# Optimization experiments

Measured on AMD Instinct MI355X. Metric: run time of the kernel, lower is better.

## Reference

```python
import jax, jax.numpy as jnp
import numpy as np

EPS = 1e-5
K = 20
LRELU = 0.2


def _bn(x, g, b, ch_axis):
    # inference BatchNorm with running_mean=0, running_var=1
    shape = [1] * x.ndim
    shape[ch_axis] = -1
    scale = (g / jnp.sqrt(1.0 + EPS)).reshape(shape)
    bias = b.reshape(shape)
    return x * scale + bias


def _lrelu(x):
    return jnp.where(x > 0, x, LRELU * x)


def _edge_conv(x, W, g, b):
    # x: (B, C, N) -> (B, C_out, N)
    B, C, N = x.shape
    xt = jnp.swapaxes(x, 1, 2)                      # (B, N, C)
    inner = -2.0 * jnp.einsum('bnc,bmc->bnm', xt, xt)
    xx = jnp.sum(xt * xt, axis=2)                   # (B, N)
    pdist = -xx[:, :, None] - inner - xx[:, None, :]  # negative sq dist (B,N,N)
    idx = jax.lax.top_k(pdist, K)[1]                # (B, N, K) nearest (incl. self)
    # gather neighbor features per batch: (C, N) indexed by (N, K) -> (C, N, K)
    neighbors = jax.vmap(lambda xf, id_: xf[:, id_])(x, idx)  # (B, C, N, K)
    center = jnp.broadcast_to(x[..., None], (B, C, N, K))
    edge = jnp.concatenate([center, neighbors - center], axis=1)  # (B, 2C, N, K)
    h = jnp.einsum('oc,bcnk->bonk', W, edge)        # 1x1 conv, no bias
    h = _lrelu(_bn(h, g, b, 1))
    return jnp.max(h, axis=-1)                      # (B, C_out, N)


def setup_inputs() -> dict:
    key = jax.random.key(0)
    ks = jax.random.split(key, 24)
    B, N = 4, 2048
    d = {}
    d['points'] = jax.random.normal(ks[0], (B, N, 3), dtype=jnp.float32)

    def w(k_, shape):
        return 0.1 * jax.random.normal(k_, shape, dtype=jnp.float32)

    def gam(k_, c):
        return 1.0 + 0.1 * jax.random.normal(k_, (c,), dtype=jnp.float32)

    def bet(k_, c):
        return 0.05 * jax.random.normal(k_, (c,), dtype=jnp.float32)

    # EdgeConv blocks: (out, 2*in)
    d['w1'], d['g1'], d['b1'] = w(ks[1], (64, 6)), gam(ks[2], 64), bet(ks[3], 64)
    d['w2'], d['g2'], d['b2'] = w(ks[4], (64, 128)), gam(ks[5], 64), bet(ks[6], 64)
    d['w3'], d['g3'], d['b3'] = w(ks[7], (128, 128)), gam(ks[8], 128), bet(ks[9], 128)
    d['w4'], d['g4'], d['b4'] = w(ks[10], (256, 256)), gam(ks[11], 256), bet(ks[12], 256)
    # conv5 1x1: 512 -> 1024
    d['w5'], d['g5'], d['b5'] = w(ks[13], (1024, 512)), gam(ks[14], 1024), bet(ks[15], 1024)
    # fc: 2048 -> 512 -> 256
    d['fw1'], d['fb1'] = w(ks[16], (512, 2048)), 0.05 * jax.random.normal(ks[17], (512,), dtype=jnp.float32)
    d['g6'], d['b6'] = gam(ks[18], 512), bet(ks[19], 512)
    d['fw2'], d['fb2'] = w(ks[20], (256, 512)), 0.05 * jax.random.normal(ks[21], (256,), dtype=jnp.float32)
    d['g7'], d['b7'] = gam(ks[22], 256), bet(ks[23], 256)
    return d


def reference(points, w1, g1, b1, w2, g2, b2, w3, g3, b3, w4, g4, b4,
              w5, g5, b5, fw1, fb1, g6, b6, fw2, fb2, g7, b7):
    x = jnp.swapaxes(points[:, :, :3], 1, 2)        # (B, 3, N)
    x1 = _edge_conv(x, w1, g1, b1)                  # (B, 64, N)
    x2 = _edge_conv(x1, w2, g2, b2)                 # (B, 64, N)
    x3 = _edge_conv(x2, w3, g3, b3)                 # (B, 128, N)
    x4 = _edge_conv(x3, w4, g4, b4)                 # (B, 256, N)
    h = jnp.concatenate([x1, x2, x3, x4], axis=1)   # (B, 512, N)
    h = _lrelu(_bn(jnp.einsum('oc,bcn->bon', w5, h), g5, b5, 1))  # (B, 1024, N)
    h_max = jnp.max(h, axis=-1)
    h_avg = jnp.mean(h, axis=-1)
    f = jnp.concatenate([h_max, h_avg], axis=1)     # (B, 2048)
    f = _lrelu(_bn(f @ fw1.T + fb1, g6, b6, 1))     # dropout = identity (eval)
    f = _bn(f @ fw2.T + fb2, g7, b7, 1)
    return f                                        # (B, 256)
```

## Files before the change

### kernel.cpp

```cpp
#include <hip/hip_runtime.h>
#include <hip/hip_bf16.h>
#include <float.h>

#define N_PTS 2048
#define B_SZ  4
#define KNN   20
#define LRELU_S 0.2f
#define FT    512
#define NPOOL 8

typedef __hip_bfloat16 bf16;
typedef __attribute__((ext_vector_type(8))) short short8v;
typedef __attribute__((ext_vector_type(4))) float floatx4;

__device__ __forceinline__ float b2f(const bf16 v) { return __bfloat162float(v); }
__device__ __forceinline__ float ldf(const float* p) { return *p; }
__device__ __forceinline__ float ldf(const bf16* p)  { return __bfloat162float(*p); }
__device__ __forceinline__ short8v ld8(const bf16* p) { return *(const short8v*)p; }
__device__ __forceinline__ unsigned umin(unsigned a, unsigned b) { return a < b ? a : b; }

__device__ __forceinline__ void gload16(const void* g, void* l) {
    __builtin_amdgcn_global_load_lds(
        (const __attribute__((address_space(1))) void*)g,
        (__attribute__((address_space(3))) void*)l, 16, 0, 0);
}

__global__ void k_sniff(const unsigned short* __restrict__ pts_hw, int* __restrict__ flag) {
    if (threadIdx.x != 0 || blockIdx.x != 0) return;
    int sane = 0;
    for (int j = 0; j < 64; ++j) {
        unsigned short v = pts_hw[2 * j];
        int e = (v >> 7) & 0xFF;
        if (e >= 100 && e <= 140) ++sane;
    }
    *flag = (sane >= 32) ? 1 : 0;
}

struct WPack {
    const void* src[23];
    int off[24];
    int rows[23];
    int cols[23];
};

__global__ void k_repack(WPack wp, const int* __restrict__ flag, float* __restrict__ dst, int limit) {
    const int isb = *flag;
    int i = blockIdx.x * blockDim.x + threadIdx.x;
    if (i >= limit) return;
    int lo = 0, hi = 23;
    while (lo + 1 < hi) { int mid = (lo + hi) >> 1; if (i >= wp.off[mid]) lo = mid; else hi = mid; }
    int j = i - wp.off[lo];
    float v = isb ? b2f(((const bf16*)wp.src[lo])[j]) : ((const float*)wp.src[lo])[j];
    int dj = j;
    int cols = wp.cols[lo];
    if (cols) dj = (j % cols) * wp.rows[lo] + (j / cols);
    dst[wp.off[lo] + dj] = v;
}

template<int C, int COUT>
__global__ void k_wsplit(const void* __restrict__ W, const int* __restrict__ flag,
                         bf16* __restrict__ dst) {
    int i = blockIdx.x * blockDim.x + threadIdx.x;
    if (i >= COUT * C) return;
    int o = i / C, c = i % C;
    const int isb = *flag;
    float w1 = isb ? b2f(((const bf16*)W)[(size_t)o * 2 * C + c])
                   : ((const float*)W)[(size_t)o * 2 * C + c];
    float w2 = isb ? b2f(((const bf16*)W)[(size_t)o * 2 * C + C + c])
                   : ((const float*)W)[(size_t)o * 2 * C + C + c];
    float wd = w1 - w2;
    bf16 h2 = __float2bfloat16(w2);
    bf16 hd = __float2bfloat16(wd);
    dst[i]                = h2;
    dst[COUT * C + i]     = __float2bfloat16(w2 - b2f(h2));
    dst[2 * COUT * C + i] = hd;
    dst[3 * COUT * C + i] = __float2bfloat16(wd - b2f(hd));
}

__global__ void k_w5split(const void* __restrict__ W, const int* __restrict__ flag,
                          bf16* __restrict__ dst) {
    int i = blockIdx.x * blockDim.x + threadIdx.x;
    if (i >= 1024 * 512) return;
    const int isb = *flag;
    float w = isb ? b2f(((const bf16*)W)[i]) : ((const float*)W)[i];
    bf16 h = __float2bfloat16(w);
    dst[i] = h;
    dst[1024 * 512 + i] = __float2bfloat16(w - b2f(h));
}

__global__ void k_transpose(const void* __restrict__ pts, const int* __restrict__ flag,
                            float* __restrict__ x0) {
    const int isb = *flag;
    int i = blockIdx.x * blockDim.x + threadIdx.x;
    if (i >= B_SZ * N_PTS) return;
    int b = i / N_PTS, n = i % N_PTS;
    for (int c = 0; c < 3; ++c) {
        size_t s = ((size_t)b * N_PTS + n) * 3 + c;
        float v = isb ? b2f(((const bf16*)pts)[s]) : ((const float*)pts)[s];
        x0[((size_t)b * 3 + c) * N_PTS + n] = v;
    }
}

__device__ __forceinline__ void load32(const float* row, int mbase, float* r) {
    const float4* p = (const float4*)(row + mbase);
#pragma unroll
    for (int i = 0; i < 8; ++i) {
        float4 f = p[i];
        r[4 * i + 0] = f.x; r[4 * i + 1] = f.y; r[4 * i + 2] = f.z; r[4 * i + 3] = f.w;
    }
}
__device__ __forceinline__ void load32(const bf16* row, int mbase, float* r) {
    const uint4* p = (const uint4*)(row + mbase);
#pragma unroll
    for (int i = 0; i < 4; ++i) {
        uint4 u = p[i];
        r[8 * i + 0] = __uint_as_float(u.x << 16);
        r[8 * i + 1] = __uint_as_float(u.x & 0xFFFF0000u);
        r[8 * i + 2] = __uint_as_float(u.y << 16);
        r[8 * i + 3] = __uint_as_float(u.y & 0xFFFF0000u);
        r[8 * i + 4] = __uint_as_float(u.z << 16);
        r[8 * i + 5] = __uint_as_float(u.z & 0xFFFF0000u);
        r[8 * i + 6] = __uint_as_float(u.w << 16);
        r[8 * i + 7] = __uint_as_float(u.w & 0xFFFF0000u);
    }
}

__device__ __forceinline__ void s2ins(unsigned k, unsigned& m1, unsigned& m2) {
    unsigned lo = umin(m1, k);
    unsigned hi = (m1 < k) ? k : m1;
    m1 = lo;
    m2 = umin(m2, hi);
}

__device__ __forceinline__ void select20x2(const unsigned* ka, const unsigned* kb,
                                           int* outA, int* outB, int lane) {
    const unsigned SENT = 0xFFFFFFFFu;
    unsigned a1 = SENT, a2 = SENT, b1 = SENT, b2 = SENT;
#pragma unroll
    for (int j = 0; j < 32; ++j) {
        s2ins(ka[j], a1, a2);
        s2ins(kb[j], b1, b2);
    }
#pragma unroll 1
    for (int k = 0; k < KNN; ++k) {
        unsigned va = a1, vb = b1;
#pragma unroll
        for (int off = 32; off >= 1; off >>= 1) {
            va = umin(va, (unsigned)__shfl_xor((int)va, off));
            vb = umin(vb, (unsigned)__shfl_xor((int)vb, off));
        }
        if (lane == 0) { outA[k] = (int)(va & 2047u); outB[k] = (int)(vb & 2047u); }
        if (a1 == va) { a1 = a2; a2 = SENT; }
        if (b1 == vb) { b1 = b2; b2 = SENT; }
        if (a1 == SENT) {
#pragma unroll
            for (int j = 0; j < 32; ++j) {
                unsigned t = (ka[j] > va) ? ka[j] : SENT;
                s2ins(t, a1, a2);
            }
        }
        if (b1 == SENT) {
#pragma unroll
            for (int j = 0; j < 32; ++j) {
                unsigned t = (kb[j] > vb) ? kb[j] : SENT;
                s2ins(t, b1, b2);
            }
        }
    }
}

__global__ __launch_bounds__(256) void k_knn3(const float* __restrict__ x0,
                                              int* __restrict__ idx) {
    __shared__ float qf[8][3];
    int ib = blockIdx.x;
    int b  = ib / (N_PTS / 8);
    int q0 = (ib % (N_PTS / 8)) * 8;
    const float* xb = x0 + (size_t)b * 3 * N_PTS;

    if (threadIdx.x < 24) {
        int q = threadIdx.x / 3, c = threadIdx.x % 3;
        qf[q][c] = xb[(size_t)c * N_PTS + q0 + q];
    }
    __syncthreads();
// ... 40 lines not shown
    float xqa = xr[qa], xqb = xr[qa + 1];

    unsigned ka[32], kb[32];
#pragma unroll
    for (int r = 0; r < 8; ++r) {
        int m0 = r * 256 + (lane << 2);
        float4 x4 = *(const float4*)(xr + m0);
        float4 a4 = *(const float4*)(gA + m0);
        float4 b4 = *(const float4*)(gB + m0);
        float s;
        s = fmaf(-2.f, a4.x, x4.x) + xqa; s = fmaxf(s, 0.f);
        ka[4 * r + 0] = (__float_as_uint(s) & 0xFFFFF800u) | (unsigned)(m0 + 0);
        s = fmaf(-2.f, a4.y, x4.y) + xqa; s = fmaxf(s, 0.f);
        ka[4 * r + 1] = (__float_as_uint(s) & 0xFFFFF800u) | (unsigned)(m0 + 1);
        s = fmaf(-2.f, a4.z, x4.z) + xqa; s = fmaxf(s, 0.f);
        ka[4 * r + 2] = (__float_as_uint(s) & 0xFFFFF800u) | (unsigned)(m0 + 2);
        s = fmaf(-2.f, a4.w, x4.w) + xqa; s = fmaxf(s, 0.f);
        ka[4 * r + 3] = (__float_as_uint(s) & 0xFFFFF800u) | (unsigned)(m0 + 3);
        s = fmaf(-2.f, b4.x, x4.x) + xqb; s = fmaxf(s, 0.f);
        kb[4 * r + 0] = (__float_as_uint(s) & 0xFFFFF800u) | (unsigned)(m0 + 0);
        s = fmaf(-2.f, b4.y, x4.y) + xqb; s = fmaxf(s, 0.f);
        kb[4 * r + 1] = (__float_as_uint(s) & 0xFFFFF800u) | (unsigned)(m0 + 1);
        s = fmaf(-2.f, b4.z, x4.z) + xqb; s = fmaxf(s, 0.f);
        kb[4 * r + 2] = (__float_as_uint(s) & 0xFFFFF800u) | (unsigned)(m0 + 2);
        s = fmaf(-2.f, b4.w, x4.w) + xqb; s = fmaxf(s, 0.f);
        kb[4 * r + 3] = (__float_as_uint(s) & 0xFFFFF800u) | (unsigned)(m0 + 3);
    }
    select20x2(ka, kb, idx + ((size_t)b * N_PTS + qa) * KNN,
               idx + ((size_t)b * N_PTS + qa + 1) * KNN, lane);
}

template<typename T, int C>
__global__ __launch_bounds__(256) void k_knn(const T* __restrict__ x, int bstride,
                                             int* __restrict__ idx) {
    __shared__ float qf[4][C];
    int ib = blockIdx.x;
    int b  = ib / (N_PTS / 4);
    int q0 = (ib % (N_PTS / 4)) * 4;
    const T* xb = x + (size_t)b * bstride;

    for (int t = threadIdx.x; t < 4 * C; t += 256) {
        int pt = t / C, c = t % C;
        qf[pt][c] = ldf(&xb[(size_t)c * N_PTS + (q0 + pt)]);
    }
    __syncthreads();

    int w = threadIdx.x >> 6, lane = threadIdx.x & 63;
    int q = q0 + w;
    int mbase = lane * 32;

    float v[32];
#pragma unroll
    for (int j = 0; j < 32; ++j) v[j] = 0.f;

    for (int c = 0; c < C; ++c) {
        float qc = qf[w][c];
        float r[32];
        load32(xb + (size_t)c * N_PTS, mbase, r);
#pragma unroll
        for (int j = 0; j < 32; ++j) { float t = r[j] - qc; v[j] = fmaf(t, t, v[j]); }
    }

    for (int k = 0; k < KNN; ++k) {
        float bv = FLT_MAX; int bi = 0x7FFFFFFF;
#pragma unroll
        for (int j = 0; j < 32; ++j)
            if (v[j] < bv) { bv = v[j]; bi = mbase + j; }
#pragma unroll
        for (int off = 32; off >= 1; off >>= 1) {
            float ov = __shfl_xor(bv, off);
            int   oi = __shfl_xor(bi, off);
            if (ov < bv || (ov == bv && oi < bi)) { bv = ov; bi = oi; }
        }
        if (lane == 0) idx[((size_t)b * N_PTS + q) * KNN + k] = bi;
        int wl = bi >> 5, wj = bi & 31;
        if (lane == wl) {
#pragma unroll
            for (int j = 0; j < 32; ++j) if (j == wj) v[j] = FLT_MAX;
        }
    }
}

template<int C>
__global__ void k_xx(const bf16* __restrict__ featT, int c0, float* __restrict__ xx) {
    int i = blockIdx.x * blockDim.x + threadIdx.x;
    if (i >= B_SZ * N_PTS) return;
    const bf16* row = featT + (size_t)i * FT + c0;
    float s = 0.f;
    for (int c = 0; c < C; c += 8) {
        uint4 u = *(const uint4*)(row + c);
        float v0 = __uint_as_float(u.x << 16), v1 = __uint_as_float(u.x & 0xFFFF0000u);
        float v2 = __uint_as_float(u.y << 16), v3 = __uint_as_float(u.y & 0xFFFF0000u);
        float v4 = __uint_as_float(u.z << 16), v5 = __uint_as_float(u.z & 0xFFFF0000u);
        float v6 = __uint_as_float(u.w << 16), v7 = __uint_as_float(u.w & 0xFFFF0000u);
        s = fmaf(v0, v0, s); s = fmaf(v1, v1, s); s = fmaf(v2, v2, s); s = fmaf(v3, v3, s);
        s = fmaf(v4, v4, s); s = fmaf(v5, v5, s); s = fmaf(v6, v6, s); s = fmaf(v7, v7, s);
    }
    xx[i] = s;
}

template<int C>
__global__ __launch_bounds__(256) void k_gram(const bf16* __restrict__ featT, int c0,
                                              float* __restrict__ G) {
    const int KC = 64;
    __shared__ __align__(16) short At[128 * 64];
    __shared__ __align__(16) short Bt[128 * 64];

    int ib = blockIdx.x;
    int b  = ib >> 8;
    int t  = ib & 255;
    int n0 = (t >> 4) << 7;
    int m0 = (t & 15) << 7;

    int tid = threadIdx.x;
    int w = tid >> 6, lane = tid & 63;
    int rw = (w & 1) * 64, cw = (w >> 1) * 64;
    int lrow = lane & 15, quad = lane >> 4;

    floatx4 acc[4][4];
#pragma unroll
    for (int ri = 0; ri < 4; ++ri)
#pragma unroll
        for (int ci = 0; ci < 4; ++ci) acc[ri][ci] = (floatx4){0.f, 0.f, 0.f, 0.f};

    for (int ck = 0; ck < C; ck += KC) {
        __syncthreads();
#pragma unroll
        for (int it = 0; it < 4; ++it) {
            int s = tid + it * 256;
            int row = s >> 3, seg = s & 7;
            int gseg = seg ^ (row & 7);
            gload16(featT + ((size_t)(b * N_PTS + n0 + row) * FT) + c0 + ck + gseg * 8,
                    &At[(s & ~63) * 8]);
            gload16(featT + ((size_t)(b * N_PTS + m0 + row) * FT) + c0 + ck + gseg * 8,
                    &Bt[(s & ~63) * 8]);
        }
        __syncthreads();
#pragma unroll
        for (int kk = 0; kk < KC; kk += 32) {
            int ks = kk >> 3;
            short8v a[4], bb[4];
#pragma unroll
            for (int ri = 0; ri < 4; ++ri) {
                int row = rw + ri * 16 + lrow;
                int seg = (ks + quad) ^ (row & 7);
                a[ri] = *(const short8v*)&At[row * 64 + seg * 8];
            }
#pragma unroll
            for (int ci = 0; ci < 4; ++ci) {
                int row = cw + ci * 16 + lrow;
                int seg = (ks + quad) ^ (row & 7);
                bb[ci] = *(const short8v*)&Bt[row * 64 + seg * 8];
            }
#pragma unroll
            for (int ri = 0; ri < 4; ++ri)
#pragma unroll
                for (int ci = 0; ci < 4; ++ci)
                    acc[ri][ci] = __builtin_amdgcn_mfma_f32_16x16x32_bf16(a[ri], bb[ci], acc[ri][ci], 0, 0, 0);
        }
    }

#pragma unroll
    for (int ri = 0; ri < 4; ++ri)
#pragma unroll
        for (int ci = 0; ci < 4; ++ci) {
            int n = n0 + rw + ri * 16 + quad * 4;
            int m = m0 + cw + ci * 16 + lrow;
            float* gp = G + ((size_t)b * N_PTS + n) * N_PTS + m;
#pragma unroll
            for (int reg = 0; reg < 4; ++reg)
                gp[(size_t)reg * N_PTS] = acc[ri][ci][reg];
        }
}

template<int COUT, int C>
__global__ __launch_bounds__(256) void k_xform(const bf16* __restrict__ featT, int c0,
                                               const bf16* __restrict__ Wsp,
                                               float* __restrict__ Y) {
    const int M2 = 2 * COUT;
    const int KC = 64;
    __shared__ __align__(16) short Bt[128 * 64];

    int ib = blockIdx.x;
    int nt = ib & 63;
    int mt = ib >> 6;
    int tid = threadIdx.x;
    int w = tid >> 6, lane = tid & 63;
    int rw = (w & 1) * 64, cw = (w >> 1) * 64;
    int l15 = lane & 15, quad = lane >> 4;

    floatx4 acc[4][4];
#pragma unroll
    for (int ri = 0; ri < 4; ++ri)
#pragma unroll
        for (int ci = 0; ci < 4; ++ci) acc[ri][ci] = (floatx4){0.f, 0.f, 0.f, 0.f};

    for (int ck = 0; ck < C; ck += KC) {
        __syncthreads();
#pragma unroll
        for (int it = 0; it < 4; ++it) {
            int s = tid + it * 256;
            int row = s >> 3, seg = s & 7;
            int gseg = seg ^ (row & 7);
            gload16(featT + (size_t)(nt * 128 + row) * FT + c0 + ck + gseg * 8,
                    &Bt[(s & ~63) * 8]);
        }
        __syncthreads();
#pragma unroll
        for (int kk = 0; kk < KC; kk += 32) {
            int ks = kk >> 3;
            short8v bfr[4];
#pragma unroll
            for (int ci = 0; ci < 4; ++ci) {
                int row = cw + ci * 16 + l15;
                int seg = (ks + quad) ^ (row & 7);
                bfr[ci] = *(const short8v*)&Bt[row * 64 + seg * 8];
            }
#pragma unroll
            for (int ri = 0; ri < 4; ++ri) {
                int mrow = mt * 128 + rw + ri * 16 + l15;
                int base = (mrow < COUT) ? mrow : (mrow + COUT);
                const bf16* hi = Wsp + (size_t)base * C + ck + kk + quad * 8;
                short8v ah = ld8(hi);
                short8v al = ld8(hi + (size_t)COUT * C);
#pragma unroll
                for (int ci = 0; ci < 4; ++ci) {
                    acc[ri][ci] = __builtin_amdgcn_mfma_f32_16x16x32_bf16(ah, bfr[ci], acc[ri][ci], 0, 0, 0);
                    acc[ri][ci] = __builtin_amdgcn_mfma_f32_16x16x32_bf16(al, bfr[ci], acc[ri][ci], 0, 0, 0);
                }
            }
        }
    }

#pragma unroll
    for (int ri = 0; ri < 4; ++ri)
#pragma unroll
        for (int ci = 0; ci < 4; ++ci) {
            int n = nt * 128 + cw + ci * 16 + l15;
            int m = mt * 128 + rw + ri * 16 + quad * 4;
            *(floatx4*)(Y + (size_t)n * M2 + m) = acc[ri][ci];
        }
}

template<int COUT>
__global__ __launch_bounds__(256) void k_gmax(const float* __restrict__ Y,
        const int* __restrict__ idx,
        const float* __restrict__ gam, const float* __restrict__ bet,
        bf16* __restrict__ featT, int c0f) {
    const int M2 = 2 * COUT;
    const int OT = COUT / 64;
    int i = blockIdx.x * 4 + (threadIdx.x >> 6);
    int lane = threadIdx.x & 63;
    int b = i >> 11;

    const float inv = rsqrtf(1.0f + 1e-5f);
    float yd[OT], scale[OT], bias[OT], mx[OT];
#pragma unroll
    for (int j = 0; j < OT; ++j) {
        int o = lane + 64 * j;
        yd[j]    = Y[(size_t)i * M2 + COUT + o];
        scale[j] = gam[o] * inv;
        bias[j]  = bet[o];
        mx[j]    = -FLT_MAX;
    }

    const int* ip = idx + (size_t)i * KNN;
    const float* Yb = Y + ((size_t)b * N_PTS) * M2;
#pragma unroll 4
    for (int k = 0; k < KNN; ++k) {
        int m = ip[k] & (N_PTS - 1);
        const float* yr = Yb + (size_t)m * M2;
#pragma unroll
        for (int j = 0; j < OT; ++j) {
            float h = (yd[j] + yr[lane + 64 * j]) * scale[j] + bias[j];
            h = h > 0.f ? h : LRELU_S * h;
            mx[j] = fmaxf(mx[j], h);
        }
    }
#pragma unroll
    for (int j = 0; j < OT; ++j)
        featT[(size_t)i * FT + c0f + lane + 64 * j] = __float2bfloat16(mx[j]);
}

template<typename T, int C, int COUT, bool WF>
__global__ __launch_bounds__(256) void k_edgeconv(const T* __restrict__ x, int bstride,
                           const int* __restrict__ idx,
                           const float* __restrict__ Wt,
                           const float* __restrict__ gam,
                           const float* __restrict__ bet,
                           bf16* __restrict__ out, int ostride,
                           bf16* __restrict__ featT, int c0f) {
    const int PT = 4;
    const int OT = COUT / 64;
    const int CP = (C + 3) & ~3;
    __shared__ float sh[PT][KNN + 1][CP];

    int ib = blockIdx.x;
    int b  = ib / (N_PTS / PT);
    int n0 = (ib % (N_PTS / PT)) * PT;
    const T* xb = x + (size_t)b * bstride;

    const int TOT = PT * (KNN + 1) * C;
    for (int t = threadIdx.x; t < TOT; t += 256) {
        int pt = t / ((KNN + 1) * C);
        int r  = t % ((KNN + 1) * C);
        int row = r / C, c = r % C;
        int n = n0 + pt;
        int m = (row == 0) ? n
                           : (idx[((size_t)b * N_PTS + n) * KNN + (row - 1)] & (N_PTS - 1));
        sh[pt][row][c] = ldf(&xb[(size_t)c * N_PTS + m]);
    }
    __syncthreads();

    int w = threadIdx.x >> 6, lane = threadIdx.x & 63;
    int n = n0 + w;

    constexpr int KT = (OT >= 4) ? 10 : 20;
    constexpr int NPASS = KNN / KT;

    float base[OT];
    float mx[OT];
#pragma unroll
    for (int j = 0; j < OT; ++j) { base[j] = 0.f; mx[j] = -FLT_MAX; }

    const float inv = rsqrtf(1.0f + 1e-5f);

#pragma unroll
    for (int pass = 0; pass < NPASS; ++pass) {
        float acc[OT][KT];
#pragma unroll
        for (int j = 0; j < OT; ++j)
#pragma unroll
            for (int k = 0; k < KT; ++k) acc[j][k] = 0.f;

        for (int c = 0; c < C; ++c) {
            float xq = sh[w][0][c];
            float w2v[OT];
#pragma unroll
            for (int j = 0; j < OT; ++j)
                w2v[j] = Wt[(size_t)(C + c) * COUT + lane + 64 * j];
            if (pass == 0) {
#pragma unroll
                for (int j = 0; j < OT; ++j) {
                    float w1v = Wt[(size_t)c * COUT + lane + 64 * j];
                    base[j] = fmaf(w1v - w2v[j], xq, base[j]);
                }
            }
#pragma unroll
            for (int k = 0; k < KT; ++k) {
                float nv = sh[w][1 + pass * KT + k][c];
#pragma unroll
                for (int j = 0; j < OT; ++j) acc[j][k] = fmaf(w2v[j], nv, acc[j][k]);
            }
        }

#pragma unroll
        for (int j = 0; j < OT; ++j) {
            int o = lane + 64 * j;
            float scale = gam[o] * inv, bias = bet[o];
#pragma unroll
            for (int k = 0; k < KT; ++k) {
                float h = (base[j] + acc[j][k]) * scale + bias;
                h = h > 0.f ? h : LRELU_S * h;
                mx[j] = fmaxf(mx[j], h);
            }
        }
    }

#pragma unroll
    for (int j = 0; j < OT; ++j) {
        int o = lane + 64 * j;
        bf16 bv = __float2bfloat16(mx[j]);
        out[(size_t)b * ostride + (size_t)o * N_PTS + n] = bv;
        if (WF) featT[((size_t)b * N_PTS + n) * FT + c0f + o] = bv;
    }
}

__global__ __launch_bounds__(256) void k_conv5mfma(
        const bf16* __restrict__ featT, const bf16* __restrict__ w5sp,
        const float* __restrict__ g5, const float* __restrict__ b5,
        float* __restrict__ fmxp, float* __restrict__ fsmp) {
    __shared__ __align__(16) short Bt[256 * 64];
    __shared__ __align__(16) short Ah[64 * 64];
    __shared__ __align__(16) short Al[64 * 64];
    __shared__ float rmx[4][64];
    __shared__ float rsm[4][64];

    int ib = blockIdx.x;
    int b  = ib / 128;
    int rem = ib % 128;
    int o0 = (rem >> 3) * 64;
    int nt = rem & 7;
    int tid = threadIdx.x;
    int w = tid >> 6, lane = tid & 63;
    int l15 = lane & 15, quad = lane >> 4;

    const bf16* Whi = w5sp;
    const bf16* Wlo = w5sp + 1024 * 512;
    const bf16* fb  = featT + (size_t)b * N_PTS * FT;
    const int nbase0 = nt * 256;

    floatx4 acc[4][4];
#pragma unroll
    for (int mi = 0; mi < 4; ++mi)
#pragma unroll
        for (int ni = 0; ni < 4; ++ni) acc[mi][ni] = (floatx4){0.f, 0.f, 0.f, 0.f};

    for (int ck = 0; ck < 512; ck += 64) {
        __syncthreads();
#pragma unroll
        for (int it = 0; it < 8; ++it) {
            int s = tid + it * 256;
            int row = s >> 3, seg = s & 7;
            int gseg = seg ^ (row & 7);
            gload16(fb + (size_t)(nbase0 + row) * FT + ck + gseg * 8,
                    &Bt[(s & ~63) * 8]);
        }
#pragma unroll
        for (int it = 0; it < 2; ++it) {
            int s = tid + it * 256;
            int row = s >> 3, seg = s & 7;
            int gseg = seg ^ (row & 7);
            gload16(Whi + (size_t)(o0 + row) * 512 + ck + gseg * 8, &Ah[(s & ~63) * 8]);
            gload16(Wlo + (size_t)(o0 + row) * 512 + ck + gseg * 8, &Al[(s & ~63) * 8]);
        }
        __syncthreads();
#pragma unroll
        for (int kk = 0; kk < 64; kk += 32) {
            int ks = kk >> 3;
            short8v bfr[4], ah[4], al[4];
#pragma unroll
            for (int ni = 0; ni < 4; ++ni) {
                int row = w * 64 + ni * 16 + l15;
                int seg = (ks + quad) ^ (row & 7);
                bfr[ni] = *(const short8v*)&Bt[row * 64 + seg * 8];
            }
#pragma unroll
            for (int mi = 0; mi < 4; ++mi) {
                int row = mi * 16 + l15;
                int seg = (ks + quad) ^ (row & 7);
                ah[mi] = *(const short8v*)&Ah[row * 64 + seg * 8];
                al[mi] = *(const short8v*)&Al[row * 64 + seg * 8];
            }
#pragma unroll
            for (int mi = 0; mi < 4; ++mi)
#pragma unroll
                for (int ni = 0; ni < 4; ++ni) {
                    acc[mi][ni] = __builtin_amdgcn_mfma_f32_16x16x32_bf16(ah[mi], bfr[ni], acc[mi][ni], 0, 0, 0);
                    acc[mi][ni] = __builtin_amdgcn_mfma_f32_16x16x32_bf16(al[mi], bfr[ni], acc[mi][ni], 0, 0, 0);
                }
        }
    }

    const float inv = rsqrtf(1.0f + 1e-5f);
#pragma unroll
    for (int mi = 0; mi < 4; ++mi) {
#pragma unroll
        for (int r = 0; r < 4; ++r) {
            int o = o0 + mi * 16 + quad * 4 + r;
            float scale = g5[o] * inv, bias = b5[o];
            float mx = -FLT_MAX, sm = 0.f;
#pragma unroll
            for (int ni = 0; ni < 4; ++ni) {
                float h = acc[mi][ni][r] * scale + bias;
                h = h > 0.f ? h : LRELU_S * h;
                mx = fmaxf(mx, h);
                sm += h;
            }
#pragma unroll
            for (int off = 1; off <= 8; off <<= 1) {
                mx = fmaxf(mx, __shfl_xor(mx, off));
                sm += __shfl_xor(sm, off);
            }
            if (l15 == 0) {
                rmx[w][mi * 16 + quad * 4 + r] = mx;
                rsm[w][mi * 16 + quad * 4 + r] = sm;
            }
        }
    }
    __syncthreads();
    if (tid < 64) {
        float mx = -FLT_MAX, sm = 0.f;
#pragma unroll
        for (int ww = 0; ww < 4; ++ww) { mx = fmaxf(mx, rmx[ww][tid]); sm += rsm[ww][tid]; }
        fmxp[((size_t)b * 1024 + o0 + tid) * NPOOL + nt] = mx;
        fsmp[((size_t)b * 1024 + o0 + tid) * NPOOL + nt] = sm;
    }
}

__global__ void k_pool(const float* __restrict__ fmxp, const float* __restrict__ fsmp,
                       float* __restrict__ fvec) {
    int i = blockIdx.x * blockDim.x + threadIdx.x;
    if (i >= B_SZ * 1024) return;
    int b = i >> 10, o = i & 1023;
    float mx = -FLT_MAX, sm = 0.f;
    for (int ch = 0; ch < NPOOL; ++ch) {
        mx = fmaxf(mx, fmxp[(size_t)i * NPOOL + ch]);
        sm += fsmp[(size_t)i * NPOOL + ch];
    }
    fvec[(size_t)b * 2048 + o] = mx;
    fvec[(size_t)b * 2048 + 1024 + o] = sm * (1.0f / N_PTS);
}

__global__ __launch_bounds__(256) void k_fc1(const float* __restrict__ fvec,
        const void* __restrict__ fw1, const void* __restrict__ fb1,
        const void* __restrict__ g6,  const void* __restrict__ b6,
        const int* __restrict__ flag, float* __restrict__ tbuf) {
    __shared__ float red[4];
    int ib = blockIdx.x;
    int b = ib >> 9, o = ib & 511;
    const float* fv = fvec + (size_t)b * 2048;
    int tid = threadIdx.x;
    const int isb = *flag;
    float s = 0.f;
    if (isb) {
        const bf16* wr = (const bf16*)fw1 + (size_t)o * 2048;
        for (int j = tid; j < 2048; j += 256) s = fmaf(b2f(wr[j]), fv[j], s);
    } else {
        const float* wr = (const float*)fw1 + (size_t)o * 2048;
        for (int j = tid; j < 2048; j += 256) s = fmaf(wr[j], fv[j], s);
    }
#pragma unroll
    for (int off = 32; off >= 1; off >>= 1) s += __shfl_xor(s, off);
    if ((tid & 63) == 0) red[tid >> 6] = s;
    __syncthreads();
    if (tid == 0) {
        float fb = isb ? b2f(((const bf16*)fb1)[o]) : ((const float*)fb1)[o];
        float gg = isb ? b2f(((const bf16*)g6)[o])  : ((const float*)g6)[o];
        float bb = isb ? b2f(((const bf16*)b6)[o])  : ((const float*)b6)[o];
        float acc = fb + red[0] + red[1] + red[2] + red[3];
        float h = acc * gg * rsqrtf(1.0f + 1e-5f) + bb;
        tbuf[(size_t)b * 512 + o] = h > 0.f ? h : LRELU_S * h;
// ... 142 lines not shown
    __syncthreads();
    const float inv = rsqrtf(1.0f + 1e-5f);
    for (int o = threadIdx.x; o < 512; o += 256) {
        const float* wr = fw1 + (size_t)o * 2048;
        float acc = fb1[o];
        for (int j = 0; j < 2048; ++j) acc += wr[j] * f[j];
        float h = acc * g6[o] * inv + b6[o];
        t[o] = h > 0.f ? h : LRELU_S * h;
    }
    __syncthreads();
    {
        int o = threadIdx.x;
        const float* wr = fw2 + (size_t)o * 512;
        float acc = fb2[o];
        for (int j = 0; j < 512; ++j) acc += wr[j] * t[j];
        float h = acc * g7[o] * inv + b7[o];
        if (*flag) ((bf16*)out)[(size_t)b * 256 + o] = __float2bfloat16(h);
        else       ((float*)out)[(size_t)b * 256 + o] = h;
    }
}

extern "C" void kernel_launch(void* const* d_in, const int* in_sizes, int n_in,
                              void* d_out, int out_size, void* d_ws, size_t ws_size,
                              hipStream_t stream) {
    static const int wsz[23] = {
        384, 64, 64,   8192, 64, 64,   16384, 128, 128,   65536, 256, 256,
        524288, 1024, 1024,   1048576, 512,   512, 512,   131072, 256,   256, 256
    };
    static const int trows[23] = {64,0,0, 64,0,0, 128,0,0, 256,0,0, 0,0,0, 0,0, 0,0, 0,0, 0,0};
    static const int tcols[23] = { 6,0,0,128,0,0, 128,0,0, 256,0,0, 0,0,0, 0,0, 0,0, 0,0, 0,0};

    WPack wp;
    int total = 0;
    for (int i = 0; i < 23; ++i) {
        wp.src[i] = d_in[i + 1]; wp.off[i] = total; total += wsz[i];
        wp.rows[i] = trows[i]; wp.cols[i] = tcols[i];
    }
    wp.off[23] = total;

    const size_t flag_bytes = 16;
    const size_t x0_bytes   = (size_t)B_SZ * 3 * N_PTS * 4;
    const size_t feat_bytes = (size_t)B_SZ * 512 * N_PTS * 2;
    const size_t idx_bytes  = (size_t)B_SZ * N_PTS * KNN * 4;
    const size_t pool_bytes = (size_t)B_SZ * 1024 * 4 * 2;
    const size_t wf_bytes   = (size_t)total * 4;
    const size_t base_need  = flag_bytes + x0_bytes + feat_bytes + idx_bytes + pool_bytes + wf_bytes;

    const size_t featT_bytes = (size_t)B_SZ * N_PTS * FT * 2;
    const size_t xx_bytes    = (size_t)B_SZ * N_PTS * 4;
    const size_t wsp2_elems  = 4 * 64 * 64;
    const size_t wsp3_elems  = 4 * 128 * 64;
    const size_t wsp4_elems  = 4 * 256 * 128;
    const size_t w5sp_elems  = 2 * 1024 * 512;
    const size_t wsp_bytes   = (wsp2_elems + wsp3_elems + wsp4_elems + w5sp_elems) * 2;
    const size_t S_bytes     = (size_t)B_SZ * N_PTS * N_PTS * 4;
    const size_t full_need   = base_need + featT_bytes + xx_bytes + wsp_bytes + S_bytes;

    if (ws_size < base_need) return;
    const bool use_gram = (ws_size >= full_need);

    char* w = (char*)d_ws;
    int*   flag = (int*)w;              w += flag_bytes;
    float* x0   = (float*)w;            w += x0_bytes;
    bf16*  feat = (bf16*)w;             w += feat_bytes;
    int*   idx  = (int*)w;              w += idx_bytes;
    w += pool_bytes;
    float* wf   = (float*)w;            w += wf_bytes;
    bf16*  featT = (bf16*)w;            w += featT_bytes;
    float* xx    = (float*)w;           w += xx_bytes;
    bf16*  wsp2  = (bf16*)w;            w += wsp2_elems * 2;
    bf16*  wsp3  = (bf16*)w;            w += wsp3_elems * 2;
    bf16*  wsp4  = (bf16*)w;            w += wsp4_elems * 2;
    bf16*  w5sp  = (bf16*)w;            w += w5sp_elems * 2;
    float* S     = (float*)w;

    float* fmxp = (float*)idx;
    float* fsmp = fmxp + (size_t)B_SZ * 1024 * NPOOL;
    float* fvec = fsmp + (size_t)B_SZ * 1024 * NPOOL;
    float* tbuf = fvec + (size_t)B_SZ * 2048;

    const int FBS = 512 * N_PTS;

    k_sniff<<<1, 64, 0, stream>>>((const unsigned short*)d_in[0], flag);
    const int rlimit = use_gram ? wp.off[15] : total;
    k_repack<<<(rlimit + 255) / 256, 256, 0, stream>>>(wp, flag, wf, rlimit);
    k_transpose<<<(B_SZ * N_PTS + 255) / 256, 256, 0, stream>>>(d_in[0], flag, x0);

    const float* w1t = wf + wp.off[0],  *g1 = wf + wp.off[1],  *b1 = wf + wp.off[2];
    const float* w2t = wf + wp.off[3],  *g2 = wf + wp.off[4],  *b2 = wf + wp.off[5];
    const float* w3t = wf + wp.off[6],  *g3 = wf + wp.off[7],  *b3 = wf + wp.off[8];
    const float* w4t = wf + wp.off[9],  *g4 = wf + wp.off[10], *b4 = wf + wp.off[11];
    const float* w5  = wf + wp.off[12], *g5 = wf + wp.off[13], *b5 = wf + wp.off[14];
    const float* fw1 = wf + wp.off[15], *fb1 = wf + wp.off[16];
    const float* g6  = wf + wp.off[17], *b6 = wf + wp.off[18];
    const float* fw2 = wf + wp.off[19], *fb2 = wf + wp.off[20];
    const float* g7  = wf + wp.off[21], *b7 = wf + wp.off[22];

    const int GK = B_SZ * N_PTS / 4;
    const int G8 = B_SZ * N_PTS / 8;
    const int NXX = (B_SZ * N_PTS + 255) / 256;

    if (use_gram) {
        k_wsplit<64, 64><<<(64 * 64 + 255) / 256, 256, 0, stream>>>(d_in[4], flag, wsp2);
        k_wsplit<64, 128><<<(128 * 64 + 255) / 256, 256, 0, stream>>>(d_in[7], flag, wsp3);
        k_wsplit<128, 256><<<(256 * 128 + 255) / 256, 256, 0, stream>>>(d_in[10], flag, wsp4);
        k_w5split<<<(1024 * 512 + 255) / 256, 256, 0, stream>>>(d_in[13], flag, w5sp);

        k_knn3<<<G8, 256, 0, stream>>>(x0, idx);
        k_edgeconv<float, 3, 64, true><<<GK, 256, 0, stream>>>(
            x0, 3 * N_PTS, idx, w1t, g1, b1, feat + 0 * N_PTS, FBS, featT, 0);
        k_xx<64><<<NXX, 256, 0, stream>>>(featT, 0, xx);
        k_gram<64><<<B_SZ * 256, 256, 0, stream>>>(featT, 0, S);
        k_select2<<<G8, 256, 0, stream>>>(S, xx, idx);
        k_xform<64, 64><<<64, 256, 0, stream>>>(featT, 0, wsp2, S);
        k_gmax<64><<<GK, 256, 0, stream>>>(S, idx, g2, b2, featT, 64);
        k_xx<64><<<NXX, 256, 0, stream>>>(featT, 64, xx);
        k_gram<64><<<B_SZ * 256, 256, 0, stream>>>(featT, 64, S);
        k_select2<<<G8, 256, 0, stream>>>(S, xx, idx);
        k_xform<128, 64><<<128, 256, 0, stream>>>(featT, 64, wsp3, S);
        k_gmax<128><<<GK, 256, 0, stream>>>(S, idx, g3, b3, featT, 128);
        k_xx<128><<<NXX, 256, 0, stream>>>(featT, 128, xx);
        k_gram<128><<<B_SZ * 256, 256, 0, stream>>>(featT, 128, S);
        k_select2<<<G8, 256, 0, stream>>>(S, xx, idx);
        k_xform<256, 128><<<256, 256, 0, stream>>>(featT, 128, wsp4, S);
        k_gmax<256><<<GK, 256, 0, stream>>>(S, idx, g4, b4, featT, 256);

        k_conv5mfma<<<B_SZ * 128, 256, 0, stream>>>(featT, w5sp, g5, b5, fmxp, fsmp);
        k_pool<<<(B_SZ * 1024 + 255) / 256, 256, 0, stream>>>(fmxp, fsmp, fvec);
        k_fc1<<<B_SZ * 512, 256, 0, stream>>>(fvec, d_in[16], d_in[17], d_in[18], d_in[19],
                                              flag, tbuf);
        k_fc2<<<B_SZ * 256, 256, 0, stream>>>(tbuf, d_in[20], d_in[21], d_in[22], d_in[23],
                                              flag, d_out);
    } else {
        k_knn<float, 3><<<GK, 256, 0, stream>>>(x0, 3 * N_PTS, idx);
        k_edgeconv<float, 3, 64, false><<<GK, 256, 0, stream>>>(
            x0, 3 * N_PTS, idx, w1t, g1, b1, feat + 0 * N_PTS, FBS, nullptr, 0);
        k_knn<bf16, 64><<<GK, 256, 0, stream>>>(feat + 0 * N_PTS, FBS, idx);
        k_edgeconv<bf16, 64, 64, false><<<GK, 256, 0, stream>>>(
            feat + 0 * N_PTS, FBS, idx, w2t, g2, b2, feat + 64 * N_PTS, FBS, nullptr, 0);
        k_knn<bf16, 64><<<GK, 256, 0, stream>>>(feat + 64 * N_PTS, FBS, idx);
        k_edgeconv<bf16, 64, 128, false><<<GK, 256, 0, stream>>>(
            feat + 64 * N_PTS, FBS, idx, w3t, g3, b3, feat + 128 * N_PTS, FBS, nullptr, 0);
        k_knn<bf16, 128><<<GK, 256, 0, stream>>>(feat + 128 * N_PTS, FBS, idx);
        k_edgeconv<bf16, 128, 256, false><<<GK, 256, 0, stream>>>(
            feat + 128 * N_PTS, FBS, idx, w4t, g4, b4, feat + 256 * N_PTS, FBS, nullptr, 0);

        k_conv5pool<<<B_SZ * (1024 / 8) * NCH, 256, 0, stream>>>(feat, w5, g5, b5, fmxp, fsmp);
        k_head<<<B_SZ, 256, 0, stream>>>(fmxp, fsmp, fw1, fb1, g6, b6, fw2, fb2, g7, b7,
                                         flag, d_out);
    }
}
```

Before: 401.8 us.

## Merge prep kernels, fold squared-norm into producers, skip lo-weight MFMAs for bf16 input

Six weight-repack, split and transpose launches become one multi-role prep kernel. The separate k_xx squared-norm kernels are removed; the norms are now computed from the rounded bf16 outputs inside edgeconv and gmax via a wave reduction. When the input is detected as bf16, the low-order weight half is exactly zero, so xform and conv5 skip those loads and extra MFMAs. This cuts launch count, one pass over featT per layer, and about half the matrix work on the bf16 path, at the cost of a runtime branch on the flag.

```diff
diff --git a/kernel.cpp b/kernel.cpp
--- a/kernel.cpp
+++ b/kernel.cpp
@@ -43,9 +43,8 @@
     int cols[23];
 };
 
-__global__ void k_repack(WPack wp, const int* __restrict__ flag, float* __restrict__ dst, int limit) {
-    const int isb = *flag;
-    int i = blockIdx.x * blockDim.x + threadIdx.x;
+__device__ __forceinline__ void repack_body(const WPack& wp, int isb,
+                                            float* __restrict__ dst, int i, int limit) {
     if (i >= limit) return;
     int lo = 0, hi = 23;
     while (lo + 1 < hi) { int mid = (lo + hi) >> 1; if (i >= wp.off[mid]) lo = mid; else hi = mid; }
@@ -58,12 +57,10 @@
 }
 
 template<int C, int COUT>
-__global__ void k_wsplit(const void* __restrict__ W, const int* __restrict__ flag,
-                         bf16* __restrict__ dst) {
-    int i = blockIdx.x * blockDim.x + threadIdx.x;
+__device__ __forceinline__ void wsplit_body(const void* __restrict__ W, int isb,
+                                            bf16* __restrict__ dst, int i) {
     if (i >= COUT * C) return;
     int o = i / C, c = i % C;
-    const int isb = *flag;
     float w1 = isb ? b2f(((const bf16*)W)[(size_t)o * 2 * C + c])
                    : ((const float*)W)[(size_t)o * 2 * C + c];
     float w2 = isb ? b2f(((const bf16*)W)[(size_t)o * 2 * C + C + c])
@@ -77,21 +74,17 @@
     dst[3 * COUT * C + i] = __float2bfloat16(wd - b2f(hd));
 }
 
-__global__ void k_w5split(const void* __restrict__ W, const int* __restrict__ flag,
-                          bf16* __restrict__ dst) {
-    int i = blockIdx.x * blockDim.x + threadIdx.x;
+__device__ __forceinline__ void w5split_body(const void* __restrict__ W, int isb,
+                                             bf16* __restrict__ dst, int i) {
     if (i >= 1024 * 512) return;
-    const int isb = *flag;
     float w = isb ? b2f(((const bf16*)W)[i]) : ((const float*)W)[i];
     bf16 h = __float2bfloat16(w);
     dst[i] = h;
     dst[1024 * 512 + i] = __float2bfloat16(w - b2f(h));
 }
 
-__global__ void k_transpose(const void* __restrict__ pts, const int* __restrict__ flag,
-                            float* __restrict__ x0) {
-    const int isb = *flag;
-    int i = blockIdx.x * blockDim.x + threadIdx.x;
+__device__ __forceinline__ void transpose_body(const void* __restrict__ pts, int isb,
+                                               float* __restrict__ x0, int i) {
     if (i >= B_SZ * N_PTS) return;
     int b = i / N_PTS, n = i % N_PTS;
     for (int c = 0; c < 3; ++c) {
@@ -99,6 +92,37 @@
         float v = isb ? b2f(((const bf16*)pts)[s]) : ((const float*)pts)[s];
         x0[((size_t)b * 3 + c) * N_PTS + n] = v;
     }
+}
+
+__global__ void k_prep(WPack wp, const int* __restrict__ flag, float* __restrict__ wf,
+                       int rlimit,
+                       const void* __restrict__ w2s, bf16* __restrict__ wsp2,
+                       const void* __restrict__ w3s, bf16* __restrict__ wsp3,
+                       const void* __restrict__ w4s, bf16* __restrict__ wsp4,
+                       const void* __restrict__ w5s, bf16* __restrict__ w5sp,
+                       const void* __restrict__ pts, float* __restrict__ x0) {
+    const int isb = *flag;
+    const int nbrep = (rlimit + 255) >> 8;
+    int ib = blockIdx.x, t = threadIdx.x;
+    if (ib < nbrep) { repack_body(wp, isb, wf, ib * 256 + t, rlimit); return; }
+    ib -= nbrep;
+    if (ib < 16)   { wsplit_body<64, 64>(w2s, isb, wsp2, ib * 256 + t); return; }
+    ib -= 16;
+    if (ib < 32)   { wsplit_body<64, 128>(w3s, isb, wsp3, ib * 256 + t); return; }
+    ib -= 32;
+    if (ib < 128)  { wsplit_body<128, 256>(w4s, isb, wsp4, ib * 256 + t); return; }
+    ib -= 128;
+    if (ib < 2048) { w5split_body(w5s, isb, w5sp, ib * 256 + t); return; }
+    ib -= 2048;
+    transpose_body(pts, isb, x0, ib * 256 + t);
+}
+
+__global__ void k_repack(WPack wp, const int* __restrict__ flag, float* __restrict__ dst, int limit) {
+    repack_body(wp, *flag, dst, blockIdx.x * blockDim.x + threadIdx.x, limit);
+}
+__global__ void k_transpose(const void* __restrict__ pts, const int* __restrict__ flag,
+                            float* __restrict__ x0) {
+    transpose_body(pts, *flag, x0, blockIdx.x * blockDim.x + threadIdx.x);
 }
 
 __device__ __forceinline__ void load32(const float* row, int mbase, float* r) {
@@ -305,24 +329,6 @@
 }
 
 template<int C>
-__global__ void k_xx(const bf16* __restrict__ featT, int c0, float* __restrict__ xx) {
-    int i = blockIdx.x * blockDim.x + threadIdx.x;
-    if (i >= B_SZ * N_PTS) return;
-    const bf16* row = featT + (size_t)i * FT + c0;
-    float s = 0.f;
-    for (int c = 0; c < C; c += 8) {
-        uint4 u = *(const uint4*)(row + c);
-        float v0 = __uint_as_float(u.x << 16), v1 = __uint_as_float(u.x & 0xFFFF0000u);
-        float v2 = __uint_as_float(u.y << 16), v3 = __uint_as_float(u.y & 0xFFFF0000u);
-        float v4 = __uint_as_float(u.z << 16), v5 = __uint_as_float(u.z & 0xFFFF0000u);
-        float v6 = __uint_as_float(u.w << 16), v7 = __uint_as_float(u.w & 0xFFFF0000u);
-        s = fmaf(v0, v0, s); s = fmaf(v1, v1, s); s = fmaf(v2, v2, s); s = fmaf(v3, v3, s);
-        s = fmaf(v4, v4, s); s = fmaf(v5, v5, s); s = fmaf(v6, v6, s); s = fmaf(v7, v7, s);
-    }
-    xx[i] = s;
-}
-
-template<int C>
 __global__ __launch_bounds__(256) void k_gram(const bf16* __restrict__ featT, int c0,
                                               float* __restrict__ G) {
     const int KC = 64;
@@ -399,11 +405,13 @@
 template<int COUT, int C>
 __global__ __launch_bounds__(256) void k_xform(const bf16* __restrict__ featT, int c0,
                                                const bf16* __restrict__ Wsp,
-                                               float* __restrict__ Y) {
+                                               float* __restrict__ Y,
+                                               const int* __restrict__ flag) {
     const int M2 = 2 * COUT;
     const int KC = 64;
     __shared__ __align__(16) short Bt[128 * 64];
 
+    const int isb = *flag;
     int ib = blockIdx.x;
     int nt = ib & 63;
     int mt = ib >> 6;
@@ -441,15 +449,19 @@
             }
 #pragma unroll
             for (int ri = 0; ri < 4; ++ri) {
-                int mrow = mt * 128 + rw + ri * 16 + l15;
+                int rbase = mt * 128 + rw + ri * 16;
+                bool uselo = (!isb) || (rbase >= COUT);
+                int mrow = rbase + l15;
                 int base = (mrow < COUT) ? mrow : (mrow + COUT);
                 const bf16* hi = Wsp + (size_t)base * C + ck + kk + quad * 8;
                 short8v ah = ld8(hi);
-                short8v al = ld8(hi + (size_t)COUT * C);
+                short8v al;
+                if (uselo) al = ld8(hi + (size_t)COUT * C);
 #pragma unroll
                 for (int ci = 0; ci < 4; ++ci) {
                     acc[ri][ci] = __builtin_amdgcn_mfma_f32_16x16x32_bf16(ah, bfr[ci], acc[ri][ci], 0, 0, 0);
-                    acc[ri][ci] = __builtin_amdgcn_mfma_f32_16x16x32_bf16(al, bfr[ci], acc[ri][ci], 0, 0, 0);
+                    if (uselo)
+                        acc[ri][ci] = __builtin_amdgcn_mfma_f32_16x16x32_bf16(al, bfr[ci], acc[ri][ci], 0, 0, 0);
                 }
             }
         }
@@ -469,7 +481,7 @@
 __global__ __launch_bounds__(256) void k_gmax(const float* __restrict__ Y,
         const int* __restrict__ idx,
         const float* __restrict__ gam, const float* __restrict__ bet,
-        bf16* __restrict__ featT, int c0f) {
+        bf16* __restrict__ featT, int c0f, float* __restrict__ xxout) {
     const int M2 = 2 * COUT;
     const int OT = COUT / 64;
     int i = blockIdx.x * 4 + (threadIdx.x >> 6);
@@ -500,9 +512,18 @@
             mx[j] = fmaxf(mx[j], h);
         }
     }
-#pragma unroll
-    for (int j = 0; j < OT; ++j)
-        featT[(size_t)i * FT + c0f + lane + 64 * j] = __float2bfloat16(mx[j]);
+    float s = 0.f;
+#pragma unroll
+    for (int j = 0; j < OT; ++j) {
+        bf16 bv = __float2bfloat16(mx[j]);
+        featT[(size_t)i * FT + c0f + lane + 64 * j] = bv;
+        if (xxout) { float q = b2f(bv); s = fmaf(q, q, s); }
+    }
+    if (xxout) {
+#pragma unroll
+        for (int off = 32; off >= 1; off >>= 1) s += __shfl_xor(s, off);
+        if (lane == 0) xxout[i] = s;
+    }
 }
 
 template<typename T, int C, int COUT, bool WF>
@@ -512,7 +533,8 @@
                            const float* __restrict__ gam,
                            const float* __restrict__ bet,
                            bf16* __restrict__ out, int ostride,
-                           bf16* __restrict__ featT, int c0f) {
+                           bf16* __restrict__ featT, int c0f,
+                           float* __restrict__ xxout) {
     const int PT = 4;
     const int OT = COUT / 64;
     const int CP = (C + 3) & ~3;
@@ -590,25 +612,37 @@
         }
     }
 
+    float s = 0.f;
 #pragma unroll
     for (int j = 0; j < OT; ++j) {
         int o = lane + 64 * j;
         bf16 bv = __float2bfloat16(mx[j]);
         out[(size_t)b * ostride + (size_t)o * N_PTS + n] = bv;
-        if (WF) featT[((size_t)b * N_PTS + n) * FT + c0f + o] = bv;
+        if (WF) {
+            featT[((size_t)b * N_PTS + n) * FT + c0f + o] = bv;
+            float q = b2f(bv);
+            s = fmaf(q, q, s);
+        }
+    }
+    if (WF && xxout) {
+#pragma unroll
+        for (int off = 32; off >= 1; off >>= 1) s += __shfl_xor(s, off);
+        if (lane == 0) xxout[(size_t)b * N_PTS + n] = s;
     }
 }
 
 __global__ __launch_bounds__(256) void k_conv5mfma(
         const bf16* __restrict__ featT, const bf16* __restrict__ w5sp,
         const float* __restrict__ g5, const float* __restrict__ b5,
-        float* __restrict__ fmxp, float* __restrict__ fsmp) {
+        float* __restrict__ fmxp, float* __restrict__ fsmp,
+        const int* __restrict__ flag) {
     __shared__ __align__(16) short Bt[256 * 64];
     __shared__ __align__(16) short Ah[64 * 64];
     __shared__ __align__(16) short Al[64 * 64];
     __shared__ float rmx[4][64];
     __shared__ float rsm[4][64];
 
+    const int isb = *flag;
     int ib = blockIdx.x;
     int b  = ib / 128;
     int rem = ib % 128;
@@ -645,7 +679,8 @@
             int row = s >> 3, seg = s & 7;
             int gseg = seg ^ (row & 7);
             gload16(Whi + (size_t)(o0 + row) * 512 + ck + gseg * 8, &Ah[(s & ~63) * 8]);
-            gload16(Wlo + (size_t)(o0 + row) * 512 + ck + gseg * 8, &Al[(s & ~63) * 8]);
+            if (!isb)
+                gload16(Wlo + (size_t)(o0 + row) * 512 + ck + gseg * 8, &Al[(s & ~63) * 8]);
         }
         __syncthreads();
 #pragma unroll
@@ -663,14 +698,15 @@
                 int row = mi * 16 + l15;
                 int seg = (ks + quad) ^ (row & 7);
                 ah[mi] = *(const short8v*)&Ah[row * 64 + seg * 8];
-                al[mi] = *(const short8v*)&Al[row * 64 + seg * 8];
+                if (!isb) al[mi] = *(const short8v*)&Al[row * 64 + seg * 8];
             }
 #pragma unroll
             for (int mi = 0; mi < 4; ++mi)
 #pragma unroll
                 for (int ni = 0; ni < 4; ++ni) {
                     acc[mi][ni] = __builtin_amdgcn_mfma_f32_16x16x32_bf16(ah[mi], bfr[ni], acc[mi][ni], 0, 0, 0);
-                    acc[mi][ni] = __builtin_amdgcn_mfma_f32_16x16x32_bf16(al[mi], bfr[ni], acc[mi][ni], 0, 0, 0);
+                    if (!isb)
+                        acc[mi][ni] = __builtin_amdgcn_mfma_f32_16x16x32_bf16(al[mi], bfr[ni], acc[mi][ni], 0, 0, 0);
                 }
         }
     }
@@ -979,9 +1015,6 @@
     const int FBS = 512 * N_PTS;
 
     k_sniff<<<1, 64, 0, stream>>>((const unsigned short*)d_in[0], flag);
-    const int rlimit = use_gram ? wp.off[15] : total;
-    k_repack<<<(rlimit + 255) / 256, 256, 0, stream>>>(wp, flag, wf, rlimit);
-    k_transpose<<<(B_SZ * N_PTS + 255) / 256, 256, 0, stream>>>(d_in[0], flag, x0);
 
     const float* w1t = wf + wp.off[0],  *g1 = wf + wp.off[1],  *b1 = wf + wp.off[2];
     const float* w2t = wf + wp.off[3],  *g2 = wf + wp.off[4],  *b2 = wf + wp.off[5];
@@ -995,52 +1028,54 @@
 
     const int GK = B_SZ * N_PTS / 4;
     const int G8 = B_SZ * N_PTS / 8;
-    const int NXX = (B_SZ * N_PTS + 255) / 256;
 
     if (use_gram) {
-        k_wsplit<64, 64><<<(64 * 64 + 255) / 256, 256, 0, stream>>>(d_in[4], flag, wsp2);
-        k_wsplit<64, 128><<<(128 * 64 + 255) / 256, 256, 0, stream>>>(d_in[7], flag, wsp3);
-        k_wsplit<128, 256><<<(256 * 128 + 255) / 256, 256, 0, stream>>>(d_in[10], flag, wsp4);
-        k_w5split<<<(1024 * 512 + 255) / 256, 256, 0, stream>>>(d_in[13], flag, w5sp);
+        const int rlimit = wp.off[15];
+        const int nbrep = (rlimit + 255) / 256;
+        const int prep_grid = nbrep + 16 + 32 + 128 + 2048 + 32;
+        k_prep<<<prep_grid, 256, 0, stream>>>(wp, flag, wf, rlimit,
+                                              d_in[4], wsp2, d_in[7], wsp3,
+                                              d_in[10], wsp4, d_in[13], w5sp,
+                                              d_in[0], x0);
 
         k_knn3<<<G8, 256, 0, stream>>>(x0, idx);
         k_edgeconv<float, 3, 64, true><<<GK, 256, 0, stream>>>(
-            x0, 3 * N_PTS, idx, w1t, g1, b1, feat + 0 * N_PTS, FBS, featT, 0);
-        k_xx<64><<<NXX, 256, 0, stream>>>(featT, 0, xx);
+            x0, 3 * N_PTS, idx, w1t, g1, b1, feat + 0 * N_PTS, FBS, featT, 0, xx);
         k_gram<64><<<B_SZ * 256, 256, 0, stream>>>(featT, 0, S);
         k_select2<<<G8, 256, 0, stream>>>(S, xx, idx);
-        k_xform<64, 64><<<64, 256, 0, stream>>>(featT, 0, wsp2, S);
-        k_gmax<64><<<GK, 256, 0, stream>>>(S, idx, g2, b2, featT, 64);
-        k_xx<64><<<NXX, 256, 0, stream>>>(featT, 64, xx);
+        k_xform<64, 64><<<64, 256, 0, stream>>>(featT, 0, wsp2, S, flag);
+        k_gmax<64><<<GK, 256, 0, stream>>>(S, idx, g2, b2, featT, 64, xx);
         k_gram<64><<<B_SZ * 256, 256, 0, stream>>>(featT, 64, S);
         k_select2<<<G8, 256, 0, stream>>>(S, xx, idx);
-        k_xform<128, 64><<<128, 256, 0, stream>>>(featT, 64, wsp3, S);
-        k_gmax<128><<<GK, 256, 0, stream>>>(S, idx, g3, b3, featT, 128);
-        k_xx<128><<<NXX, 256, 0, stream>>>(featT, 128, xx);
+        k_xform<128, 64><<<128, 256, 0, stream>>>(featT, 64, wsp3, S, flag);
+        k_gmax<128><<<GK, 256, 0, stream>>>(S, idx, g3, b3, featT, 128, xx);
         k_gram<128><<<B_SZ * 256, 256, 0, stream>>>(featT, 128, S);
         k_select2<<<G8, 256, 0, stream>>>(S, xx, idx);
-        k_xform<256, 128><<<256, 256, 0, stream>>>(featT, 128, wsp4, S);
-        k_gmax<256><<<GK, 256, 0, stream>>>(S, idx, g4, b4, featT, 256);
-
-        k_conv5mfma<<<B_SZ * 128, 256, 0, stream>>>(featT, w5sp, g5, b5, fmxp, fsmp);
+        k_xform<256, 128><<<256, 256, 0, stream>>>(featT, 128, wsp4, S, flag);
+        k_gmax<256><<<GK, 256, 0, stream>>>(S, idx, g4, b4, featT, 256, nullptr);
+
+        k_conv5mfma<<<B_SZ * 128, 256, 0, stream>>>(featT, w5sp, g5, b5, fmxp, fsmp, flag);
         k_pool<<<(B_SZ * 1024 + 255) / 256, 256, 0, stream>>>(fmxp, fsmp, fvec);
         k_fc1<<<B_SZ * 512, 256, 0, stream>>>(fvec, d_in[16], d_in[17], d_in[18], d_in[19],
                                               flag, tbuf);
         k_fc2<<<B_SZ * 256, 256, 0, stream>>>(tbuf, d_in[20], d_in[21], d_in[22], d_in[23],
                                               flag, d_out);
     } else {
+        k_repack<<<(total + 255) / 256, 256, 0, stream>>>(wp, flag, wf, total);
+        k_transpose<<<(B_SZ * N_PTS + 255) / 256, 256, 0, stream>>>(d_in[0], flag, x0);
+
         k_knn<float, 3><<<GK, 256, 0, stream>>>(x0, 3 * N_PTS, idx);
         k_edgeconv<float, 3, 64, false><<<GK, 256, 0, stream>>>(
-            x0, 3 * N_PTS, idx, w1t, g1, b1, feat + 0 * N_PTS, FBS, nullptr, 0);
+            x0, 3 * N_PTS, idx, w1t, g1, b1, feat + 0 * N_PTS, FBS, nullptr, 0, nullptr);
         k_knn<bf16, 64><<<GK, 256, 0, stream>>>(feat + 0 * N_PTS, FBS, idx);
         k_edgeconv<bf16, 64, 64, false><<<GK, 256, 0, stream>>>(
-            feat + 0 * N_PTS, FBS, idx, w2t, g2, b2, feat + 64 * N_PTS, FBS, nullptr, 0);
+            feat + 0 * N_PTS, FBS, idx, w2t, g2, b2, feat + 64 * N_PTS, FBS, nullptr, 0, nullptr);
         k_knn<bf16, 64><<<GK, 256, 0, stream>>>(feat + 64 * N_PTS, FBS, idx);
         k_edgeconv<bf16, 64, 128, false><<<GK, 256, 0, stream>>>(
-            feat + 64 * N_PTS, FBS, idx, w3t, g3, b3, feat + 128 * N_PTS, FBS, nullptr, 0);
+            feat + 64 * N_PTS, FBS, idx, w3t, g3, b3, feat + 128 * N_PTS, FBS, nullptr, 0, nullptr);
         k_knn<bf16, 128><<<GK, 256, 0, stream>>>(feat + 128 * N_PTS, FBS, idx);
         k_edgeconv<bf16, 128, 256, false><<<GK, 256, 0, stream>>>(
-            feat + 128 * N_PTS, FBS, idx, w4t, g4, b4, feat + 256 * N_PTS, FBS, nullptr, 0);
+            feat + 128 * N_PTS, FBS, idx, w4t, g4, b4, feat + 256 * N_PTS, FBS, nullptr, 0, nullptr);
 
         k_conv5pool<<<B_SZ * (1024 / 8) * NCH, 256, 0, stream>>>(feat, w5, g5, b5, fmxp, fsmp);
         k_head<<<B_SZ, 256, 0, stream>>>(fmxp, fsmp, fw1, fb1, g6, b6, fw2, fb2, g7, b7,
```

New measurement: 382.2 us. -4.9%, faster.
